# Kernel optimization log

Hardware: AMD Instinct MI355X
Metric: run time of the kernel (lower is better)

The kernel has to match this reference:

```python
import jax, jax.numpy as jnp
import numpy as np

H = 2; C = 64          # heads, hidden_channels
N = 50000; E = 800000  # nodes, edges
D = 128                # input_dim
EPS = 1e-5

def _lrelu(x, s):
    return jnp.where(x >= 0, x, s * x)

def _ln(x, g, b):
    m = x.mean(-1, keepdims=True)
    v = ((x - m) ** 2).mean(-1, keepdims=True)
    return (x - m) / jnp.sqrt(v + EPS) * g + b

def _gatv2(x_src, x_dst, src, dst, Wl, bl, Wr, br, att, Wres, bias):
    # PyG GATv2Conv: concat=False (mean over heads), residual=True, no self loops
    n = x_dst.shape[0]
    xl = (x_src @ Wl + bl).reshape(-1, H, C)  # [Ns,H,C]
    xr = (x_dst @ Wr + br).reshape(-1, H, C)  # [Nd,H,C]
    xj = xl[src]                               # [E,H,C] messages from source
    xi = xr[dst]                               # [E,H,C]
    e = _lrelu(xi + xj, 0.2)
    alpha = jnp.einsum('ehc,hc->eh', e, att)   # [E,H]
    amax = jax.lax.stop_gradient(jax.ops.segment_max(alpha, dst, num_segments=n))
    ex = jnp.exp(alpha - amax[dst])
    den = jax.ops.segment_sum(ex, dst, num_segments=n)
    a = ex / den[dst]                          # segment softmax over incoming edges
    out = jax.ops.segment_sum(xj * a[:, :, None], dst, num_segments=n)  # [Nd,H,C]
    return out.mean(axis=1) + x_dst @ Wres + bias


def setup_inputs() -> dict:
    key = jax.random.key(0)
    ks = jax.random.split(key, 40)
    d = {}
    d['x'] = jax.random.normal(ks[0], (N, D), jnp.float32)
    d['edge_index'] = jax.random.randint(ks[1], (2, E), 0, N, jnp.int32)
    i = 2
    for p, ind in (('c1d', D), ('c1t', D), ('c2d', C), ('c2t', C)):
        d[p + '_Wl'] = jax.random.normal(ks[i], (ind, H * C), jnp.float32) * 0.05; i += 1
        d[p + '_bl'] = jnp.zeros((H * C,), jnp.float32)
        d[p + '_Wr'] = jax.random.normal(ks[i], (ind, H * C), jnp.float32) * 0.05; i += 1
        d[p + '_br'] = jnp.zeros((H * C,), jnp.float32)
        d[p + '_att'] = jax.random.normal(ks[i], (H, C), jnp.float32) * 0.05; i += 1
        d[p + '_Wres'] = jax.random.normal(ks[i], (ind, C), jnp.float32) * 0.05; i += 1
        d[p + '_bias'] = jnp.zeros((C,), jnp.float32)
    d['nd_g'] = jnp.ones((C,), jnp.float32); d['nd_b'] = jnp.zeros((C,), jnp.float32)
    d['nt_g'] = jnp.ones((C,), jnp.float32); d['nt_b'] = jnp.zeros((C,), jnp.float32)
    return d


def reference(x, edge_index, c1d_Wl, c1d_bl, c1d_Wr, c1d_br, c1d_att, c1d_Wres, c1d_bias, c1t_Wl, c1t_bl, c1t_Wr, c1t_br, c1t_att, c1t_Wres, c1t_bias, c2d_Wl, c2d_bl, c2d_Wr, c2d_br, c2d_att, c2d_Wres, c2d_bias, c2t_Wl, c2t_bl, c2t_Wr, c2t_br, c2t_att, c2t_Wres, c2t_bias, nd_g, nd_b, nt_g, nt_b):
    src, dst = edge_index[0], edge_index[1]
    dep = _gatv2(x, x, src, dst, c1d_Wl, c1d_bl, c1d_Wr, c1d_br, c1d_att, c1d_Wres, c1d_bias)
    dep = _lrelu(_ln(dep, nd_g, nd_b), 0.01)
    dant = _gatv2(x, x, dst, src, c1t_Wl, c1t_bl, c1t_Wr, c1t_br, c1t_att, c1t_Wres, c1t_bias)
    dant = _lrelu(_ln(dant, nt_g, nt_b), 0.01)
    dep2 = _lrelu(_gatv2(dep, dep, src, dst, c2d_Wl, c2d_bl, c2d_Wr, c2d_br, c2d_att, c2d_Wres, c2d_bias), 0.01)
    dant2 = _lrelu(_gatv2(dant, dant, dst, src, c2t_Wl, c2t_bl, c2t_Wr, c2t_br, c2t_att, c2t_Wres, c2t_bias), 0.01)
    return jnp.concatenate([dep2, dant2, x], axis=-1)
```

## Files before the change

### kernel.cpp

```cpp
#include <hip/hip_runtime.h>
#include <math.h>

typedef unsigned short ushort_t;
typedef unsigned char uchar_t;
typedef __attribute__((ext_vector_type(8))) short short8x;
typedef __attribute__((ext_vector_type(4))) float f32x4;
typedef __attribute__((ext_vector_type(2))) float f32x2;

#define CSHIFT 9
#define CC 12288
#define EPB 4096
#define ECAP 2048
#define NCMAX 128

__device__ __forceinline__ unsigned f2bf(float f) {
  unsigned u = __float_as_uint(f);
  u += 0x7fff + ((u >> 16) & 1);
  return u >> 16;
}
__device__ __forceinline__ float bf2f(ushort_t u) {
  return __uint_as_float(((unsigned)u) << 16);
}
__device__ __forceinline__ float dpp_red8(float v) {
  v += __int_as_float(__builtin_amdgcn_update_dpp(0, __float_as_int(v), 0xB1, 0xF, 0xF, true));
  v += __int_as_float(__builtin_amdgcn_update_dpp(0, __float_as_int(v), 0x4E, 0xF, 0xF, true));
  v += __int_as_float(__builtin_amdgcn_update_dpp(0, __float_as_int(v), 0x141, 0xF, 0xF, true));
  return v;
}

struct GArgs {
  const float* Wl[2];
  const float* bl[2];
  const float* Wr[2];
  const float* br[2];
  const float* Wres[2];
  const float* bias[2];
};

__device__ __forceinline__ float wval1(const GArgs& ga, int col, int k) {
  int dir = col >= 320 ? 1 : 0;
  int cc = col - dir * 320;
  return cc < 128 ? ga.Wl[dir][k * 128 + cc]
       : cc < 256 ? ga.Wr[dir][k * 128 + (cc - 128)]
                  : ga.Wres[dir][k * 64 + (cc - 256)];
}
__device__ __forceinline__ float bval(const GArgs& ga, int col) {
  int dir = col >= 320 ? 1 : 0;
  int cc = col - dir * 320;
  return cc < 128 ? ga.bl[dir][cc]
       : cc < 256 ? ga.br[dir][cc - 128]
                  : ga.bias[dir][cc - 256];
}


__global__ __launch_bounds__(128) void pack_kernel(GArgs g1, GArgs g2,
                                                   ushort_t* __restrict__ WT1,
                                                   ushort_t* __restrict__ WT2,
                                                   float* __restrict__ bc1,
                                                   float* __restrict__ bc2) {
  int b = blockIdx.x;
  int k = threadIdx.x;
  if (b < 640) {
    WT1[b * 128 + k] = (ushort_t)f2bf(wval1(g1, b, k));
  } else if (b < 1280) {
    int c = b - 640;
    int dir = c >= 320 ? 1 : 0;
    int cc = c - dir * 320;
    float v = 0.f;
    if ((k >> 6) == dir) {
      int k2 = k & 63;
      v = cc < 128 ? g2.Wl[dir][k2 * 128 + cc]
        : cc < 256 ? g2.Wr[dir][k2 * 128 + (cc - 128)]
                   : g2.Wres[dir][k2 * 64 + (cc - 256)];
    }
    WT2[c * 128 + k] = (ushort_t)f2bf(v);
  } else {
    for (int c = k; c < 640; c += 128) {
      bc1[c] = bval(g1, c);
      bc2[c] = bval(g2, c);
    }
  }
}


template <int AF32>
__device__ __forceinline__ void gemm_body(const float* Af, const ushort_t* Ab,
                                          const ushort_t* WT, const float* bc,
                                          ushort_t* Y, uchar_t* XL8, int N,
                                          int rb, int cb, ushort_t* lds) {
  const int tid = threadIdx.x;
  const int lane = tid & 63;
  const int w = tid >> 6;
  const int m0 = rb * 64;
  const int cbase = cb * 128 + w * 32;

#pragma unroll
  for (int c = 0; c < 4; ++c) {
    int Lb = (tid + c * 256) * 16;
    int row = Lb >> 8, within = Lb & 255;
    int so = within ^ ((row & 7) << 4);
    int grow = m0 + row;
    if (grow >= N) grow = N - 1;
    if (AF32) {
      const float* src = Af + (size_t)grow * 128 + (so >> 1);
      float4 a = *(const float4*)src;
      float4 b = *(const float4*)(src + 4);
      uint4 o;
      o.x = f2bf(a.x) | (f2bf(a.y) << 16);
      o.y = f2bf(a.z) | (f2bf(a.w) << 16);
      o.z = f2bf(b.x) | (f2bf(b.y) << 16);
      o.w = f2bf(b.z) | (f2bf(b.w) << 16);
      ((uint4*)lds)[tid + c * 256] = o;
    } else {
      ((uint4*)lds)[tid + c * 256] = *(const uint4*)(Ab + (size_t)grow * 128 + (so >> 1));
    }
  }

  short8x bf[4][2];
#pragma unroll
  for (int ks = 0; ks < 4; ++ks)
#pragma unroll
    for (int ns = 0; ns < 2; ++ns) {
      int col = cbase + ns * 16 + (lane & 15);
      bf[ks][ns] = *(const short8x*)(WT + (size_t)col * 128 + ks * 32 + (lane >> 4) * 8);
    }

  __syncthreads();

  f32x4 z = {0.f, 0.f, 0.f, 0.f};
  f32x4 acc[4][2];
#pragma unroll
  for (int ms = 0; ms < 4; ++ms) {
    acc[ms][0] = z;
    acc[ms][1] = z;
  }
#pragma unroll
  for (int ks = 0; ks < 4; ++ks) {
    short8x af[4];
#pragma unroll
    for (int ms = 0; ms < 4; ++ms) {
      int row = ms * 16 + (lane & 15);
      int byte = row * 256 + ((ks * 64 + (lane >> 4) * 16) ^ ((row & 7) << 4));
      af[ms] = *(const short8x*)((const char*)lds + byte);
    }
#pragma unroll
    for (int ms = 0; ms < 4; ++ms) {
      acc[ms][0] = __builtin_amdgcn_mfma_f32_16x16x32_bf16(af[ms], bf[ks][0], acc[ms][0], 0, 0, 0);
      acc[ms][1] = __builtin_amdgcn_mfma_f32_16x16x32_bf16(af[ms], bf[ks][1], acc[ms][1], 0, 0, 0);
    }
  }

#pragma unroll
  for (int ms = 0; ms < 4; ++ms)
#pragma unroll
    for (int ns = 0; ns < 2; ++ns) {
      int col = cbase + ns * 16 + (lane & 15);
      float bv = bc[col];
      int dir = col >= 320 ? 1 : 0;
      int cc = col - dir * 320;
#pragma unroll
      for (int r = 0; r < 4; ++r) {
        int grow = m0 + ms * 16 + (lane >> 4) * 4 + r;
        if (grow < N) {
          float val = acc[ms][ns][r] + bv;
          if (cc < 128) {
            int pk = __builtin_amdgcn_cvt_pk_fp8_f32(val, val, 0, false);
            XL8[(size_t)grow * 256 + dir * 128 + cc] = (uchar_t)(pk & 0xff);
          } else {
            Y[(size_t)grow * 640 + col] = (ushort_t)f2bf(val);
          }
        }
      }
    }
}


__global__ __launch_bounds__(256) void k_front(
    const float* __restrict__ x, const int* __restrict__ ei, int E, int N,
    int* __restrict__ gc0, int* __restrict__ gc1, int* __restrict__ ctail0,
    int* __restrict__ ctail1, const ushort_t* __restrict__ WT1,
    const float* __restrict__ bc1, ushort_t* __restrict__ Y,
    uchar_t* __restrict__ XL8, float* __restrict__ out, int nbinA, int ngemm,
    int nrow) {
  __shared__ ushort_t lds[8192];
  const int bid = blockIdx.x;
  const int t = threadIdx.x;
  if (bid < nbinA) {
    int* h0 = (int*)lds;
    int* h1 = h0 + NCMAX;
    int* b0 = h1 + NCMAX;
    int* b1 = b0 + NCMAX;
    const int e0 = bid * EPB;
    const int e1 = min(e0 + EPB, E);
    for (int i = t; i < NCMAX; i += 256) {
      h0[i] = 0;
      h1[i] = 0;
    }
    __syncthreads();
    for (int i = e0 + t; i < e1; i += 256) {
      int s = ei[i], d = ei[E + i];
      atomicAdd(&h0[d >> CSHIFT], 1);
      atomicAdd(&h1[s >> CSHIFT], 1);
    }
    __syncthreads();
    for (int c = t; c < NCMAX; c += 256) {
      int n0 = h0[c], n1 = h1[c];
      b0[c] = n0 ? atomicAdd(&ctail0[c], n0) : 0;
      b1[c] = n1 ? atomicAdd(&ctail1[c], n1) : 0;
      h0[c] = 0;
      h1[c] = 0;
    }
    __syncthreads();
    for (int i = e0 + t; i < e1; i += 256) {
      int s = ei[i], d = ei[E + i];
      int c0 = d >> CSHIFT;
      int p0 = b0[c0] + atomicAdd(&h0[c0], 1);
      if (p0 < CC) gc0[c0 * CC + p0] = (s << 16) | d;
      int c1 = s >> CSHIFT;
      int p1 = b1[c1] + atomicAdd(&h1[c1], 1);
      if (p1 < CC) gc1[c1 * CC + p1] = (d << 16) | s;
    }
  } else if (bid < nbinA + ngemm) {
    int gb = bid - nbinA;
    gemm_body<1>(x, nullptr, WT1, bc1, Y, XL8, N, gb % nrow, gb / nrow, lds);
  } else {
    int i = (bid - nbinA - ngemm) * 256 + t;
    if (i < N * 32) {
      float4 v = ((const float4*)x)[i];
      ((float4*)out)[(size_t)(i >> 5) * 64 + 32 + (i & 31)] = v;
    }
  }
}


__global__ __launch_bounds__(256) void gemm2_kernel(const ushort_t* __restrict__ A,
                                                    const ushort_t* __restrict__ WT,
                                                    const float* __restrict__ bc,
                                                    ushort_t* __restrict__ Y,
                                                    uchar_t* __restrict__ XL8, int N) {
  __shared__ ushort_t lds[8192];
  gemm_body<0>(nullptr, A, WT, bc, Y, XL8, N, blockIdx.x, blockIdx.y, lds);
}


template <int MODE>
__global__ __launch_bounds__(256) void agg_bucket(
    const ushort_t* __restrict__ Y, const uchar_t* __restrict__ XL8,
    const int* __restrict__ gc0, const int* __restrict__ gc1,
    const int* __restrict__ ctail0, const int* __restrict__ ctail1,
    const float* __restrict__ attA, const float* __restrict__ attB,
    const float* __restrict__ lng0, const float* __restrict__ lnb0,
    const float* __restrict__ lng1, const float* __restrict__ lnb1,
    void* __restrict__ outp, int ncoarse, int N) {
  __shared__ ushort_t lnbr[ECAP + 24];
  __shared__ int hist[64], offs[64], cur[64];
  const int bid = blockIdx.x;
  const int xcd = bid & 7;
  const int q = bid >> 3;
  const int cb = (q >> 3) * 8 + xcd;
  const int fi = q & 7;
  if (cb >= ncoarse) return;
  const int fb = cb * 8 + fi;
  if (fb * 64 >= N) return;
  const int dir = blockIdx.y;
  const int t = threadIdx.x;
  const int* gc = dir ? gc1 : gc0;
  const int* ctail = dir ? ctail1 : ctail0;
  const float* att = dir ? attB : attA;

  for (int i = t; i < (ECAP + 24) / 2; i += 256) ((int*)lnbr)[i] = 0;
  if (t < 64) {
    hist[t] = 0;
    cur[t] = 0;
  }
  __syncthreads();

  const int cntc = min(ctail[cb], CC);
  const int* src = gc + cb * CC;
  for (int i = t; i < cntc; i += 256) {
    int e = src[i];
    if (((e & 0xFFFF) >> 6) == fb) atomicAdd(&hist[e & 63], 1);
  }
  __syncthreads();
  if (t < 64) {
    int v = hist[t], inc = v;
#pragma unroll
    for (int o = 1; o < 64; o <<= 1) {
      int u = __shfl_up(inc, o);
      if (t >= o) inc += u;
    }
    offs[t] = min(inc - v, ECAP - 1);
  }
  __syncthreads();
  for (int i = t; i < cntc; i += 256) {
    int e = src[i];
    if (((e & 0xFFFF) >> 6) == fb) {
      int r = e & 63;
      int pos = offs[r] + atomicAdd(&cur[r], 1);
      if (pos < ECAP) lnbr[pos] = (ushort_t)((unsigned)e >> 16);
    }
  }
  __syncthreads();

  const int wv = t >> 6, lane = t & 63, g = lane >> 4, jj = lane & 15;
  const float L2E = 1.4426950408889634f;
  float av[8];
  {
    float4 a0 = *(const float4*)(att + jj * 8);
    float4 a1 = *(const float4*)(att + jj * 8 + 4);
    av[0] = a0.x * L2E; av[1] = a0.y * L2E; av[2] = a0.z * L2E; av[3] = a0.w * L2E;
    av[4] = a1.x * L2E; av[5] = a1.y * L2E; av[6] = a1.z * L2E; av[7] = a1.w * L2E;
  }
  const uchar_t* X8b = XL8 + dir * 128 + jj * 8;

  for (int r = wv; r < 64; r += 4) {
    const int n = fb * 64 + r;
    if (n >= N) break;
    const char* rowp = (const char*)Y + (size_t)n * 1280 + dir * 640;

    float xi[8];
    {
      short8x v = *(const short8x*)(rowp + 256 + jj * 16);
#pragma unroll
      for (int q2 = 0; q2 < 8; ++q2) xi[q2] = bf2f((ushort_t)v[q2]);
    }
    float d = 0.f;
    float acc[8];
#pragma unroll
    for (int q2 = 0; q2 < 8; ++q2) acc[q2] = 0.f;

    const int beg = offs[r], deg = min(hist[r], ECAP - beg);
    if (deg > 0) {
      int oA = (int)lnbr[beg + g] << 8;
      int oB = (int)lnbr[beg + 4 + g] << 8;
      uint2 vC = *(const uint2*)(X8b + (size_t)(unsigned)oA);
      uint2 vD = *(const uint2*)(X8b + (size_t)(unsigned)oB);
      for (int k0 = 0; k0 < deg; k0 += 4) {
        int oN = (int)lnbr[beg + k0 + 8 + g] << 8;
        uint2 vN = *(const uint2*)(X8b + (size_t)(unsigned)oN);
        f32x2 x01 = __builtin_amdgcn_cvt_pk_f32_fp8((int)vC.x, false);
        f32x2 x23 = __builtin_amdgcn_cvt_pk_f32_fp8((int)vC.x, true);
        f32x2 x45 = __builtin_amdgcn_cvt_pk_f32_fp8((int)vC.y, false);
        f32x2 x67 = __builtin_amdgcn_cvt_pk_f32_fp8((int)vC.y, true);
        float xj[8] = {x01[0], x01[1], x23[0], x23[1],
                       x45[0], x45[1], x67[0], x67[1]};
        float p = 0.f;
#pragma unroll
        for (int q2 = 0; q2 < 8; ++q2) {
          float e = xi[q2] + xj[q2];
          e = fmaxf(e, 0.2f * e);
          p = fmaf(e, av[q2], p);
        }
        p = dpp_red8(p);
        float wgt = (k0 + g < deg) ? __builtin_amdgcn_exp2f(p) : 0.f;
        d += wgt;
#pragma unroll
        for (int q2 = 0; q2 < 8; ++q2) acc[q2] = fmaf(xj[q2], wgt, acc[q2]);
        vC = vD;
        vD = vN;
      }
#pragma unroll
      for (int o = 16; o <= 32; o <<= 1) {
        d += __shfl_xor(d, o);
#pragma unroll
        for (int q2 = 0; q2 < 8; ++q2) acc[q2] += __shfl_xor(acc[q2], o);
      }
    }
    float inv = deg > 0 ? 1.f / d : 0.f;
    float v[8];
#pragma unroll
    for (int q2 = 0; q2 < 8; ++q2) {
      float tq = acc[q2] * inv;
      v[q2] = 0.5f * (tq + __shfl_xor(tq, 8));
    }
    {
      short8x rv = *(const short8x*)(rowp + 512 + (jj & 7) * 16);
#pragma unroll
      for (int q2 = 0; q2 < 8; ++q2) v[q2] += bf2f((ushort_t)rv[q2]);
    }

    if (MODE == 0) {
      float s = 0.f;
#pragma unroll
      for (int q2 = 0; q2 < 8; ++q2) s += v[q2];
      s += __shfl_xor(s, 1);
      s += __shfl_xor(s, 2);
      s += __shfl_xor(s, 4);
      float mu = s * (1.f / 64.f);
      float vs = 0.f;
#pragma unroll
      for (int q2 = 0; q2 < 8; ++q2) {
        float dv = v[q2] - mu;
        vs += dv * dv;
      }
      vs += __shfl_xor(vs, 1);
      vs += __shfl_xor(vs, 2);
      vs += __shfl_xor(vs, 4);
      float rstd = rsqrtf(vs * (1.f / 64.f) + 1e-5f);
      if (g == 0 && jj < 8) {
        const float* lg = dir ? lng1 : lng0;
        const float* lb = dir ? lnb1 : lnb0;
        unsigned o2[8];
#pragma unroll
        for (int q2 = 0; q2 < 8; ++q2) {
          int c = jj * 8 + q2;
          float y = (v[q2] - mu) * rstd * lg[c] + lb[c];
          y = fmaxf(y, 0.01f * y);
          o2[q2] = f2bf(y);
        }
        uint4 pk;
        pk.x = o2[0] | (o2[1] << 16);
        pk.y = o2[2] | (o2[3] << 16);
        pk.z = o2[4] | (o2[5] << 16);
        pk.w = o2[6] | (o2[7] << 16);
        *(uint4*)((ushort_t*)outp + (size_t)n * 128 + dir * 64 + jj * 8) = pk;
      }
    } else {
      if (g == 0 && jj < 8) {
        float* op = (float*)outp + (size_t)n * 256 + dir * 64 + jj * 8;
        float4 o0, o1;
        o0.x = fmaxf(v[0], 0.01f * v[0]);
        o0.y = fmaxf(v[1], 0.01f * v[1]);
        o0.z = fmaxf(v[2], 0.01f * v[2]);
        o0.w = fmaxf(v[3], 0.01f * v[3]);
        o1.x = fmaxf(v[4], 0.01f * v[4]);
        o1.y = fmaxf(v[5], 0.01f * v[5]);
        o1.z = fmaxf(v[6], 0.01f * v[6]);
        o1.w = fmaxf(v[7], 0.01f * v[7]);
        *(float4*)op = o0;
        *(float4*)(op + 4) = o1;
      }
    }
  }
}


extern "C" void kernel_launch(void* const* d_in, const int* in_sizes, int n_in,
                              void* d_out, int out_size, void* d_ws, size_t ws_size,
                              hipStream_t stream) {
  const float* x = (const float*)d_in[0];
  const int* ei = (const int*)d_in[1];
  const int N = in_sizes[0] / 128;
  const int E = in_sizes[1] / 2;
  float* out = (float*)d_out;
  const int ncoarse = (N + (1 << CSHIFT) - 1) >> CSHIFT;

  char* p = (char*)d_ws;
  auto carve = [&](size_t bytes) {
    char* q = p;
    p += ((bytes + 255) & ~(size_t)255);
    return q;
  };
  int* ctail = (int*)carve(2 * NCMAX * 4);
  int* gc0 = (int*)carve((size_t)ncoarse * CC * 4);
  int* gc1 = (int*)carve((size_t)ncoarse * CC * 4);
  ushort_t* Y1 = (ushort_t*)carve((size_t)N * 640 * 2);
  uchar_t* XL8 = (uchar_t*)carve((size_t)N * 256);
  ushort_t* A2 = (ushort_t*)carve((size_t)N * 128 * 2);
  ushort_t* WT1 = (ushort_t*)carve(640 * 128 * 2);
  ushort_t* WT2 = (ushort_t*)carve(640 * 128 * 2);
  float* bc1 = (float*)carve(640 * 4);
  float* bc2 = (float*)carve(640 * 4);
  int* ctail0 = ctail;
  int* ctail1 = ctail + NCMAX;

  auto F = [&](int i) { return (const float*)d_in[i]; };
  GArgs g1, g2;
  g1.Wl[0] = F(2);  g1.bl[0] = F(3);  g1.Wr[0] = F(4);  g1.br[0] = F(5);
  g1.Wres[0] = F(7); g1.bias[0] = F(8);
  g1.Wl[1] = F(9);  g1.bl[1] = F(10); g1.Wr[1] = F(11); g1.br[1] = F(12);
  g1.Wres[1] = F(14); g1.bias[1] = F(15);
  g2.Wl[0] = F(16); g2.bl[0] = F(17); g2.Wr[0] = F(18); g2.br[0] = F(19);
  g2.Wres[0] = F(21); g2.bias[0] = F(22);
  g2.Wl[1] = F(23); g2.bl[1] = F(24); g2.Wr[1] = F(25); g2.br[1] = F(26);
  g2.Wres[1] = F(28); g2.bias[1] = F(29);

  hipMemsetAsync(ctail, 0, 2 * NCMAX * 4, stream);

  pack_kernel<<<1281, 128, 0, stream>>>(g1, g2, WT1, WT2, bc1, bc2);

  const int nbinA = (E + EPB - 1) / EPB;
  const int nrow = (N + 63) / 64;
  const int ngemm = nrow * 5;
  const int ncopy = (N * 32 + 255) / 256;
  k_front<<<nbinA + ngemm + ncopy, 256, 0, stream>>>(
      x, ei, E, N, gc0, gc1, ctail0, ctail1, WT1, bc1, Y1, XL8, out,
      nbinA, ngemm, nrow);

  const int pcb8 = ((ncoarse + 7) / 8) * 8;
  const dim3 ga(pcb8 * 8, 2);
  agg_bucket<0><<<ga, 256, 0, stream>>>(Y1, XL8, gc0, gc1, ctail0, ctail1,
                                        F(6), F(13), F(30), F(31), F(32), F(33),
                                        A2, ncoarse, N);
  gemm2_kernel<<<dim3(nrow, 5), 256, 0, stream>>>(A2, WT2, bc2, Y1, XL8, N);
  agg_bucket<1><<<ga, 256, 0, stream>>>(Y1, XL8, gc0, gc1, ctail0, ctail1,
                                        F(20), F(27), nullptr, nullptr, nullptr,
                                        nullptr, out, ncoarse, N);
}
```

Before: 312.2 us.

## Halve aggregation block node span and prefetch next node's row and neighbors

Each aggregation block now handles 32 destination nodes instead of 64, with 16 fine blocks per coarse bucket and half the LDS neighbor capacity. That doubles the grid for more parallelism and shrinks the per-block LDS footprint. The per-wave node loop is software-pipelined: the next node's xi/residual rows and its first two gathered neighbor vectors are loaded while the current node is finished. The cost is that every block rescans the whole coarse bucket, so scan work doubles. The lower ECAP also silently truncates very high-degree nodes.

Measured after the change: 350.6 us. +12.3%, slower.

```diff
diff --git a/kernel.cpp b/kernel.cpp
--- a/kernel.cpp
+++ b/kernel.cpp
@@ -10,7 +10,7 @@
 #define CSHIFT 9
 #define CC 12288
 #define EPB 4096
-#define ECAP 2048
+#define ECAP 1024
 #define NCMAX 128
 
 __device__ __forceinline__ unsigned f2bf(float f) {
@@ -252,24 +252,24 @@
     const float* __restrict__ lng0, const float* __restrict__ lnb0,
     const float* __restrict__ lng1, const float* __restrict__ lnb1,
     void* __restrict__ outp, int ncoarse, int N) {
-  __shared__ ushort_t lnbr[ECAP + 24];
-  __shared__ int hist[64], offs[64], cur[64];
+  __shared__ ushort_t lnbr[ECAP + 32];
+  __shared__ int hist[32], offs[32], cur[32];
   const int bid = blockIdx.x;
   const int xcd = bid & 7;
   const int q = bid >> 3;
-  const int cb = (q >> 3) * 8 + xcd;
-  const int fi = q & 7;
+  const int cb = (q >> 4) * 8 + xcd;
+  const int fi = q & 15;
   if (cb >= ncoarse) return;
-  const int fb = cb * 8 + fi;
-  if (fb * 64 >= N) return;
+  const int fb = cb * 16 + fi;
+  if (fb * 32 >= N) return;
   const int dir = blockIdx.y;
   const int t = threadIdx.x;
   const int* gc = dir ? gc1 : gc0;
   const int* ctail = dir ? ctail1 : ctail0;
   const float* att = dir ? attB : attA;
 
-  for (int i = t; i < (ECAP + 24) / 2; i += 256) ((int*)lnbr)[i] = 0;
-  if (t < 64) {
+  for (int i = t; i < (ECAP + 32) / 2; i += 256) ((int*)lnbr)[i] = 0;
+  if (t < 32) {
     hist[t] = 0;
     cur[t] = 0;
   }
@@ -279,13 +279,13 @@
   const int* src = gc + cb * CC;
   for (int i = t; i < cntc; i += 256) {
     int e = src[i];
-    if (((e & 0xFFFF) >> 6) == fb) atomicAdd(&hist[e & 63], 1);
+    if (((e & 0xFFFF) >> 5) == fb) atomicAdd(&hist[e & 31], 1);
   }
   __syncthreads();
-  if (t < 64) {
+  if (t < 32) {
     int v = hist[t], inc = v;
 #pragma unroll
-    for (int o = 1; o < 64; o <<= 1) {
+    for (int o = 1; o < 32; o <<= 1) {
       int u = __shfl_up(inc, o);
       if (t >= o) inc += u;
     }
@@ -294,8 +294,8 @@
   __syncthreads();
   for (int i = t; i < cntc; i += 256) {
     int e = src[i];
-    if (((e & 0xFFFF) >> 6) == fb) {
-      int r = e & 63;
+    if (((e & 0xFFFF) >> 5) == fb) {
+      int r = e & 31;
       int pos = offs[r] + atomicAdd(&cur[r], 1);
       if (pos < ECAP) lnbr[pos] = (ushort_t)((unsigned)e >> 16);
     }
@@ -313,31 +313,36 @@
   }
   const uchar_t* X8b = XL8 + dir * 128 + jj * 8;
 
-  for (int r = wv; r < 64; r += 4) {
-    const int n = fb * 64 + r;
-    if (n >= N) break;
-    const char* rowp = (const char*)Y + (size_t)n * 1280 + dir * 640;
+  int curBeg = offs[wv], curDeg = min(hist[wv], ECAP - offs[wv]);
+  int n0 = min(fb * 32 + wv, N - 1);
+  const char* rowp0 = (const char*)Y + (size_t)n0 * 1280 + dir * 640;
+  short8x xiR = *(const short8x*)(rowp0 + 256 + jj * 16);
+  short8x rvR = *(const short8x*)(rowp0 + 512 + (jj & 7) * 16);
+  uint2 vC = *(const uint2*)(X8b + ((size_t)lnbr[curBeg + g] << 8));
+  uint2 vD = *(const uint2*)(X8b + ((size_t)lnbr[curBeg + 4 + g] << 8));
+
+  for (int r = wv; r < 32; r += 4) {
+    const int n = fb * 32 + r;
+    const int rn = min(r + 4, 31);
+    const int begN = offs[rn];
+    const int degN = min(hist[rn], ECAP - begN);
+    const int nn = min(fb * 32 + rn, N - 1);
+    const char* rowpN = (const char*)Y + (size_t)nn * 1280 + dir * 640;
+    short8x xiN = *(const short8x*)(rowpN + 256 + jj * 16);
+    short8x rvN = *(const short8x*)(rowpN + 512 + (jj & 7) * 16);
 
     float xi[8];
-    {
-      short8x v = *(const short8x*)(rowp + 256 + jj * 16);
-#pragma unroll
-      for (int q2 = 0; q2 < 8; ++q2) xi[q2] = bf2f((ushort_t)v[q2]);
-    }
+#pragma unroll
+    for (int q2 = 0; q2 < 8; ++q2) xi[q2] = bf2f((ushort_t)xiR[q2]);
     float d = 0.f;
     float acc[8];
 #pragma unroll
     for (int q2 = 0; q2 < 8; ++q2) acc[q2] = 0.f;
 
-    const int beg = offs[r], deg = min(hist[r], ECAP - beg);
+    const int beg = curBeg, deg = curDeg;
     if (deg > 0) {
-      int oA = (int)lnbr[beg + g] << 8;
-      int oB = (int)lnbr[beg + 4 + g] << 8;
-      uint2 vC = *(const uint2*)(X8b + (size_t)(unsigned)oA);
-      uint2 vD = *(const uint2*)(X8b + (size_t)(unsigned)oB);
       for (int k0 = 0; k0 < deg; k0 += 4) {
-        int oN = (int)lnbr[beg + k0 + 8 + g] << 8;
-        uint2 vN = *(const uint2*)(X8b + (size_t)(unsigned)oN);
+        uint2 vN2 = *(const uint2*)(X8b + ((size_t)lnbr[beg + k0 + 8 + g] << 8));
         f32x2 x01 = __builtin_amdgcn_cvt_pk_f32_fp8((int)vC.x, false);
         f32x2 x23 = __builtin_amdgcn_cvt_pk_f32_fp8((int)vC.x, true);
         f32x2 x45 = __builtin_amdgcn_cvt_pk_f32_fp8((int)vC.y, false);
@@ -357,7 +362,7 @@
 #pragma unroll
         for (int q2 = 0; q2 < 8; ++q2) acc[q2] = fmaf(xj[q2], wgt, acc[q2]);
         vC = vD;
-        vD = vN;
+        vD = vN2;
       }
 #pragma unroll
       for (int o = 16; o <= 32; o <<= 1) {
@@ -366,6 +371,10 @@
         for (int q2 = 0; q2 < 8; ++q2) acc[q2] += __shfl_xor(acc[q2], o);
       }
     }
+
+    vC = *(const uint2*)(X8b + ((size_t)lnbr[begN + g] << 8));
+    vD = *(const uint2*)(X8b + ((size_t)lnbr[begN + 4 + g] << 8));
+
     float inv = deg > 0 ? 1.f / d : 0.f;
     float v[8];
 #pragma unroll
@@ -373,11 +382,8 @@
       float tq = acc[q2] * inv;
       v[q2] = 0.5f * (tq + __shfl_xor(tq, 8));
     }
-    {
-      short8x rv = *(const short8x*)(rowp + 512 + (jj & 7) * 16);
-#pragma unroll
-      for (int q2 = 0; q2 < 8; ++q2) v[q2] += bf2f((ushort_t)rv[q2]);
-    }
+#pragma unroll
+    for (int q2 = 0; q2 < 8; ++q2) v[q2] += bf2f((ushort_t)rvR[q2]);
 
     if (MODE == 0) {
       float s = 0.f;
@@ -397,7 +403,7 @@
       vs += __shfl_xor(vs, 2);
       vs += __shfl_xor(vs, 4);
       float rstd = rsqrtf(vs * (1.f / 64.f) + 1e-5f);
-      if (g == 0 && jj < 8) {
+      if (n < N && g == 0 && jj < 8) {
         const float* lg = dir ? lng1 : lng0;
         const float* lb = dir ? lnb1 : lnb0;
         unsigned o2[8];
@@ -416,7 +422,7 @@
         *(uint4*)((ushort_t*)outp + (size_t)n * 128 + dir * 64 + jj * 8) = pk;
       }
     } else {
-      if (g == 0 && jj < 8) {
+      if (n < N && g == 0 && jj < 8) {
         float* op = (float*)outp + (size_t)n * 256 + dir * 64 + jj * 8;
         float4 o0, o1;
         o0.x = fmaxf(v[0], 0.01f * v[0]);
@@ -431,6 +437,11 @@
         *(float4*)(op + 4) = o1;
       }
     }
+
+    curBeg = begN;
+    curDeg = degN;
+    xiR = xiN;
+    rvR = rvN;
   }
 }
 
@@ -487,8 +498,8 @@
       x, ei, E, N, gc0, gc1, ctail0, ctail1, WT1, bc1, Y1, XL8, out,
       nbinA, ngemm, nrow);
 
-  const int pcb8 = ((ncoarse + 7) / 8) * 8;
-  const dim3 ga(pcb8 * 8, 2);
+  const int ngrp = (ncoarse + 7) / 8;
+  const dim3 ga(ngrp * 128, 2);
   agg_bucket<0><<<ga, 256, 0, stream>>>(Y1, XL8, gc0, gc1, ctail0, ctail1,
                                         F(6), F(13), F(30), F(31), F(32), F(33),
                                         A2, ncoarse, N);
```
